# Optimization experiments

Hardware: AMD Instinct MI355X
Metric: run time of the kernel (lower is better)

Reference implementation:

```python
import jax, jax.numpy as jnp
import numpy as np

B, T, IN, H, OUT = 1024, 512, 16, 64, 8


def setup_inputs() -> dict:
    key = jax.random.key(0)
    ks = jax.random.split(key, 7)
    s = 1.0 / np.sqrt(H)
    return {
        "x": jax.random.normal(ks[0], (B, T, IN), dtype=jnp.float32),
        "W_ih": jax.random.normal(ks[1], (4 * H, IN), dtype=jnp.float32) * s,
        "W_hh": jax.random.normal(ks[2], (4 * H, H), dtype=jnp.float32) * s,
        "b_ih": jax.random.normal(ks[3], (4 * H,), dtype=jnp.float32) * s,
        "b_hh": jax.random.normal(ks[4], (4 * H,), dtype=jnp.float32) * s,
        "W_fc": jax.random.normal(ks[5], (OUT, H), dtype=jnp.float32) * s,
        "b_fc": jax.random.normal(ks[6], (OUT,), dtype=jnp.float32) * s,
    }


def reference(x, W_ih, W_hh, b_ih, b_hh, W_fc, b_fc):
    Bq, Tq, _ = x.shape
    Hq = W_hh.shape[1]
    # Precompute input contribution for all timesteps: [T, B, 4H]
    xw = jnp.einsum("bti,gi->tbg", x, W_ih) + b_ih + b_hh

    def step(carry, xw_t):
        h, c = carry
        gates = xw_t + h @ W_hh.T  # [B, 4H]
        i, f, g, o = jnp.split(gates, 4, axis=-1)  # PyTorch gate order i,f,g,o
        i = jax.nn.sigmoid(i)
        f = jax.nn.sigmoid(f)
        g = jnp.tanh(g)
        o = jax.nn.sigmoid(o)
        c = f * c + i * g
        h = o * jnp.tanh(c)
        return (h, c), None

    h0 = jnp.zeros((Bq, Hq), dtype=x.dtype)
    c0 = jnp.zeros((Bq, Hq), dtype=x.dtype)
    (h_last, _), _ = jax.lax.scan(step, (h0, c0), xw)

    # fc on last timestep only, then sigmoid -> [B, 1, OUT]
    out = jax.nn.sigmoid(h_last @ W_fc.T + b_fc)
    return out[:, None, :]
```

## Files before the change

### kernel.cpp

```cpp
#include <hip/hip_runtime.h>
#include <math.h>


#define LSTM_T 512
#define LSTM_IN 16
#define LSTM_H 64
#define LSTM_OUT 8
#define BT 2
#define HSTRIDE 72

#define L2E   1.44269504088896340736f
#define L2E2  2.88539008177792681472f

typedef _Float16 half8  __attribute__((ext_vector_type(8)));
typedef float    floatx4 __attribute__((ext_vector_type(4)));

static __device__ __forceinline__ float fast_rcp(float x) { return __builtin_amdgcn_rcpf(x); }
static __device__ __forceinline__ float fast_exp2(float x) { return __builtin_amdgcn_exp2f(x); }
static __device__ __forceinline__ float sigm2(float p) { return fast_rcp(1.0f + fast_exp2(-p)); }
static __device__ __forceinline__ float tanh2(float p) {
    return fmaf(-2.0f, fast_rcp(1.0f + fast_exp2(p)), 1.0f);
}
static __device__ __forceinline__ void pin4(int4& v) {
    asm volatile("" : "+v"(v.x), "+v"(v.y), "+v"(v.z), "+v"(v.w));
}
static __device__ __forceinline__ void pinf4(float4& v) {
    asm volatile("" : "+v"(v.x), "+v"(v.y), "+v"(v.z), "+v"(v.w));
}
static __device__ __forceinline__ void lite_barrier() {
    asm volatile("s_waitcnt lgkmcnt(0)\n\ts_barrier" ::: "memory");
}
static __device__ __forceinline__ unsigned pk2h(float a, float b) {
    return __builtin_bit_cast(unsigned, __builtin_amdgcn_cvt_pkrtz(a, b));
}
static __device__ __forceinline__ half8 to_h8(float4 a, float4 b) {
    uint4 u = make_uint4(pk2h(a.x, a.y), pk2h(a.z, a.w), pk2h(b.x, b.y), pk2h(b.z, b.w));
    return __builtin_bit_cast(half8, u);
}
static __device__ __forceinline__ int4 cvt8h(float4 a, float4 b, float sc) {
    float4 as = make_float4(a.x * sc, a.y * sc, a.z * sc, a.w * sc);
    float4 bs = make_float4(b.x * sc, b.y * sc, b.z * sc, b.w * sc);
    return __builtin_bit_cast(int4, to_h8(as, bs));
}
static __device__ __forceinline__ float4 ld4(const float* p) {
    return *reinterpret_cast<const float4*>(p);
}
static __device__ __forceinline__ float sel4(floatx4 v, bool r0, bool r1) {
    float lo = r0 ? v[1] : v[0];
    float hi = r0 ? v[3] : v[2];
    return r1 ? hi : lo;
}

__global__ __launch_bounds__(256, 2)
void lstm_mfma_kernel(const float* __restrict__ x,
                      const float* __restrict__ W_ih,
                      const float* __restrict__ W_hh,
                      const float* __restrict__ b_ih,
                      const float* __restrict__ b_hh,
                      const float* __restrict__ W_fc,
                      const float* __restrict__ b_fc,
                      float* __restrict__ out) {
    const int tid   = threadIdx.x;
    const int lane  = tid & 63;
    const int w     = tid >> 6;
    const int q     = lane >> 4;
    const int m     = lane & 15;
    const int b     = m & 1;
    const int rho   = (m >> 1) & 3;
    const bool r0   = (rho & 1) != 0;
    const bool r1   = (rho & 2) != 0;
    const int jmine = 16 * w + 4 * q + rho;
    const bool wr   = (m < 8);
    const int bbase = blockIdx.x * BT;

    __shared__ __align__(16) _Float16 hbuf[2][BT][HSTRIDE];
    __shared__ __align__(16) float hfin[BT][LSTM_H];

    int4 Ah[4][2], Ax[4];
    float4 bias4[4];
    #pragma unroll
    for (int tt = 0; tt < 4; ++tt) {
        const float sc = (tt == 2) ? L2E2 : L2E;
        const int gt = tt * 64 + 16 * w + m;
        #pragma unroll
        for (int c = 0; c < 2; ++c) {
            const float* s = W_hh + gt * LSTM_H + 32 * c + 8 * q;
            Ah[tt][c] = cvt8h(ld4(s), ld4(s + 4), sc);
            pin4(Ah[tt][c]);
        }
        float4 xa = make_float4(0.f, 0.f, 0.f, 0.f), xb = xa;
        if (q < 2) {
            const float* s = W_ih + gt * LSTM_IN + 8 * q;
            xa = ld4(s); xb = ld4(s + 4);
        }
        Ax[tt] = cvt8h(xa, xb, sc);
        pin4(Ax[tt]);
        const int gb = tt * 64 + 16 * w + 4 * q;
        float4 bi = ld4(b_ih + gb), bh = ld4(b_hh + gb);
        bias4[tt] = make_float4((bi.x + bh.x) * sc, (bi.y + bh.y) * sc,
                                (bi.z + bh.z) * sc, (bi.w + bh.w) * sc);
        pinf4(bias4[tt]);
    }

    if (tid < 64) {
        int bb = tid >> 5, jj = tid & 31;
        reinterpret_cast<int*>(&hbuf[0][bb][0])[jj] = 0;
    }

    const float* xp = x + (size_t)(bbase + b) * LSTM_T * LSTM_IN + 8 * q;
    float4 xA0 = make_float4(0.f, 0.f, 0.f, 0.f), xA1 = xA0;
    float4 xB0 = xA0, xB1 = xA0;
    if (q < 2) {
        xA0 = ld4(xp);              xA1 = ld4(xp + 4);
        xB0 = ld4(xp + LSTM_IN);    xB1 = ld4(xp + LSTM_IN + 4);
    }
    __syncthreads();

    float creg = 0.0f, hreg = 0.0f;

#define STEP(T_, X0, X1)                                                        \
    {                                                                           \
        const _Float16* cur = &hbuf[(T_) & 1][0][0];                            \
        _Float16*       nxt = &hbuf[((T_) + 1) & 1][0][0];                      \
                                        \
        half8 bh0 = *reinterpret_cast<const half8*>(cur + b * HSTRIDE + 8 * q); \
        half8 bh1 = *reinterpret_cast<const half8*>(cur + b * HSTRIDE + 32 + 8 * q); \
         \
        half8 xf = to_h8(X0, X1);                                               \
        floatx4 acc[4];                                                         \
        _Pragma("unroll")                                                       \
        for (int tt = 0; tt < 4; ++tt)                                          \
            acc[tt] = __builtin_amdgcn_mfma_f32_16x16x32_f16(                   \
                __builtin_bit_cast(half8, Ax[tt]), xf,                          \
                __builtin_bit_cast(floatx4, bias4[tt]), 0, 0, 0);               \
                       \
        if (q < 2 && (T_) + 2 < LSTM_T) {                                       \
            X0 = ld4(xp + (size_t)((T_) + 2) * LSTM_IN);                        \
            X1 = ld4(xp + (size_t)((T_) + 2) * LSTM_IN + 4);                    \
        }                                                                       \
        _Pragma("unroll")                                                       \
        for (int tt = 0; tt < 4; ++tt)                                          \
            acc[tt] = __builtin_amdgcn_mfma_f32_16x16x32_f16(                   \
                __builtin_bit_cast(half8, Ah[tt][0]), bh0, acc[tt], 0, 0, 0);   \
        _Pragma("unroll")                                                       \
        for (int tt = 0; tt < 4; ++tt)                                          \
            acc[tt] = __builtin_amdgcn_mfma_f32_16x16x32_f16(                   \
                __builtin_bit_cast(half8, Ah[tt][1]), bh1, acc[tt], 0, 0, 0);   \
               \
        float gi = sigm2(sel4(acc[0], r0, r1));                                 \
        float gf = sigm2(sel4(acc[1], r0, r1));                                 \
        float gg = tanh2(sel4(acc[2], r0, r1));                                 \
        float go = sigm2(sel4(acc[3], r0, r1));                                 \
        creg = fmaf(gf, creg, gi * gg);                                         \
        hreg = go * tanh2(creg * L2E2);                                         \
               \
        if (wr) nxt[b * HSTRIDE + jmine] = (_Float16)hreg;                      \
        lite_barrier();                                                         \
    }

    for (int t = 0; t < LSTM_T; t += 2) {
        STEP(t,     xA0, xA1)
        STEP(t + 1, xB0, xB1)
    }
#undef STEP

    if (wr) hfin[b][jmine] = hreg;
    __syncthreads();

    if (tid < BT * LSTM_OUT) {
        int bb = tid >> 3, o = tid & 7;
        float s = b_fc[o];
        #pragma unroll
        for (int j4 = 0; j4 < LSTM_H / 4; ++j4) {
            float4 wv = ld4(W_fc + o * LSTM_H + 4 * j4);
            float4 hv = *reinterpret_cast<const float4*>(&hfin[bb][4 * j4]);
            s = fmaf(wv.x, hv.x, s);
            s = fmaf(wv.y, hv.y, s);
            s = fmaf(wv.z, hv.z, s);
            s = fmaf(wv.w, hv.w, s);
        }
        out[(size_t)(bbase + bb) * LSTM_OUT + o] = sigm2(s * L2E);
    }
}

extern "C" void kernel_launch(void* const* d_in, const int* in_sizes, int n_in,
                              void* d_out, int out_size, void* d_ws, size_t ws_size,
                              hipStream_t stream) {
    const float* x    = (const float*)d_in[0];
    const float* W_ih = (const float*)d_in[1];
    const float* W_hh = (const float*)d_in[2];
    const float* b_ih = (const float*)d_in[3];
    const float* b_hh = (const float*)d_in[4];
    const float* W_fc = (const float*)d_in[5];
    const float* b_fc = (const float*)d_in[6];
    float* out = (float*)d_out;

    lstm_mfma_kernel<<<1024 / BT, 256, 0, stream>>>(
        x, W_ih, W_hh, b_ih, b_hh, W_fc, b_fc, out);
}
```

Measured before the change: 268.0 us.

## Split gate activations across half-waves and exchange via ds_swizzle

The log2e scaling is moved out of the weights and bias and into the activation step, so the weights are now converted to fp16 unscaled. Each lane previously computed all four gate activations itself, duplicating the work in both halves of each 16-lane group. Now one half computes f and i (sigmoid) while the other computes g (tanh) and o (sigmoid), and the results are exchanged with a ds_swizzle. This halves the transcendental work per lane on the serial critical path, but adds an LDS swizzle latency every step, and the extra scaling multiplies now happen inside the loop.

```diff
diff --git a/kernel.cpp b/kernel.cpp
--- a/kernel.cpp
+++ b/kernel.cpp
@@ -37,10 +37,8 @@
     uint4 u = make_uint4(pk2h(a.x, a.y), pk2h(a.z, a.w), pk2h(b.x, b.y), pk2h(b.z, b.w));
     return __builtin_bit_cast(half8, u);
 }
-static __device__ __forceinline__ int4 cvt8h(float4 a, float4 b, float sc) {
-    float4 as = make_float4(a.x * sc, a.y * sc, a.z * sc, a.w * sc);
-    float4 bs = make_float4(b.x * sc, b.y * sc, b.z * sc, b.w * sc);
-    return __builtin_bit_cast(int4, to_h8(as, bs));
+static __device__ __forceinline__ int4 cvt8h(float4 a, float4 b) {
+    return __builtin_bit_cast(int4, to_h8(a, b));
 }
 static __device__ __forceinline__ float4 ld4(const float* p) {
     return *reinterpret_cast<const float4*>(p);
@@ -49,6 +47,10 @@
     float lo = r0 ? v[1] : v[0];
     float hi = r0 ? v[3] : v[2];
     return r1 ? hi : lo;
+}
+static __device__ __forceinline__ float swz8(float v) {
+    int r = __builtin_amdgcn_ds_swizzle(__builtin_bit_cast(int, v), 0x201F);
+    return __builtin_bit_cast(float, r);
 }
 
 __global__ __launch_bounds__(256, 2)
@@ -69,9 +71,14 @@
     const int rho   = (m >> 1) & 3;
     const bool r0   = (rho & 1) != 0;
     const bool r1   = (rho & 2) != 0;
+    const bool h1   = (m & 8) != 0;
     const int jmine = 16 * w + 4 * q + rho;
     const bool wr   = (m < 8);
     const int bbase = blockIdx.x * BT;
+
+    const float s1 = h1 ? L2E2 : -L2E;
+    const float a1 = h1 ? 1.0f : 0.0f;
+    const float b1 = h1 ? -2.0f : 1.0f;
 
     __shared__ __align__(16) _Float16 hbuf[2][BT][HSTRIDE];
     __shared__ __align__(16) float hfin[BT][LSTM_H];
@@ -80,12 +87,11 @@
     float4 bias4[4];
     #pragma unroll
     for (int tt = 0; tt < 4; ++tt) {
-        const float sc = (tt == 2) ? L2E2 : L2E;
         const int gt = tt * 64 + 16 * w + m;
         #pragma unroll
         for (int c = 0; c < 2; ++c) {
             const float* s = W_hh + gt * LSTM_H + 32 * c + 8 * q;
-            Ah[tt][c] = cvt8h(ld4(s), ld4(s + 4), sc);
+            Ah[tt][c] = cvt8h(ld4(s), ld4(s + 4));
             pin4(Ah[tt][c]);
         }
         float4 xa = make_float4(0.f, 0.f, 0.f, 0.f), xb = xa;
@@ -93,12 +99,11 @@
             const float* s = W_ih + gt * LSTM_IN + 8 * q;
             xa = ld4(s); xb = ld4(s + 4);
         }
-        Ax[tt] = cvt8h(xa, xb, sc);
+        Ax[tt] = cvt8h(xa, xb);
         pin4(Ax[tt]);
         const int gb = tt * 64 + 16 * w + 4 * q;
         float4 bi = ld4(b_ih + gb), bh = ld4(b_hh + gb);
-        bias4[tt] = make_float4((bi.x + bh.x) * sc, (bi.y + bh.y) * sc,
-                                (bi.z + bh.z) * sc, (bi.w + bh.w) * sc);
+        bias4[tt] = make_float4(bi.x + bh.x, bi.y + bh.y, bi.z + bh.z, bi.w + bh.w);
         pinf4(bias4[tt]);
     }
 
@@ -122,10 +127,9 @@
     {                                                                           \
         const _Float16* cur = &hbuf[(T_) & 1][0][0];                            \
         _Float16*       nxt = &hbuf[((T_) + 1) & 1][0][0];                      \
-                                        \
+         \
         half8 bh0 = *reinterpret_cast<const half8*>(cur + b * HSTRIDE + 8 * q); \
         half8 bh1 = *reinterpret_cast<const half8*>(cur + b * HSTRIDE + 32 + 8 * q); \
-         \
         half8 xf = to_h8(X0, X1);                                               \
         floatx4 acc[4];                                                         \
         _Pragma("unroll")                                                       \
@@ -147,13 +151,23 @@
             acc[tt] = __builtin_amdgcn_mfma_f32_16x16x32_f16(                   \
                 __builtin_bit_cast(half8, Ah[tt][1]), bh1, acc[tt], 0, 0, 0);   \
                \
-        float gi = sigm2(sel4(acc[0], r0, r1));                                 \
-        float gf = sigm2(sel4(acc[1], r0, r1));                                 \
-        float gg = tanh2(sel4(acc[2], r0, r1));                                 \
-        float go = sigm2(sel4(acc[3], r0, r1));                                 \
-        creg = fmaf(gf, creg, gi * gg);                                         \
-        hreg = go * tanh2(creg * L2E2);                                         \
-               \
+        floatx4 v1, v2;                                                         \
+        _Pragma("unroll")                                                       \
+        for (int r = 0; r < 4; ++r) {                                           \
+            v1[r] = h1 ? acc[2][r] : acc[1][r];                                 \
+            v2[r] = h1 ? acc[3][r] : acc[0][r];                                 \
+        }                                                                       \
+        float u1 = sel4(v1, r0, r1);                                            \
+        float u2 = sel4(v2, r0, r1);                                            \
+             \
+        float act1 = fmaf(b1, fast_rcp(1.0f + fast_exp2(s1 * u1)), a1);         \
+        float act2 = fast_rcp(1.0f + fast_exp2(-L2E * u2));   \
+                \
+        float g_in = swz8(act1);                                                \
+        float o_in = swz8(act2);                                                \
+            \
+        creg = fmaf(act1, creg, act2 * g_in);                  \
+        hreg = o_in * tanh2(creg * L2E2);                      \
         if (wr) nxt[b * HSTRIDE + jmine] = (_Float16)hreg;                      \
         lite_barrier();                                                         \
     }
```

After: 260.2 us. -2.9%, faster.
